# Performance work log

Measured on AMD Instinct MI355X. Metric: run time of the kernel, lower is better.

The kernel has to match this reference:

```python
import jax, jax.numpy as jnp
import numpy as np

N_NODES = 100000
N_EDGES = 1600000
N_QUERY = 200000
IN_CH = 128
HID = 64


def setup_inputs() -> dict:
    key = jax.random.key(0)
    ks = jax.random.split(key, 8)
    x = jax.random.normal(ks[0], (N_NODES, IN_CH), dtype=jnp.float32)
    edge_index = jax.random.randint(ks[1], (2, N_EDGES), 0, N_NODES, dtype=jnp.int64)
    src = jax.random.randint(ks[2], (N_QUERY,), 0, N_NODES, dtype=jnp.int64)
    dst = jax.random.randint(ks[3], (N_QUERY,), 0, N_NODES, dtype=jnp.int64)
    # SAGEConv params: lin_l (neighbor path, with bias), lin_r (root path, no bias)
    s1 = 1.0 / np.sqrt(IN_CH)
    s2 = 1.0 / np.sqrt(HID)
    Wl1 = jax.random.normal(ks[4], (HID, IN_CH), dtype=jnp.float32) * s1
    bl1 = jnp.zeros((HID,), dtype=jnp.float32)
    Wr1 = jax.random.normal(ks[5], (HID, IN_CH), dtype=jnp.float32) * s1
    Wl2 = jax.random.normal(ks[6], (HID, HID), dtype=jnp.float32) * s2
    bl2 = jnp.zeros((HID,), dtype=jnp.float32)
    Wr2 = jax.random.normal(ks[7], (HID, HID), dtype=jnp.float32) * s2
    return {"x": x, "edge_index": edge_index, "src": src, "dst": dst,
            "Wl1": Wl1, "bl1": bl1, "Wr1": Wr1,
            "Wl2": Wl2, "bl2": bl2, "Wr2": Wr2}


def _sage_conv(h, edge_src, edge_dst, Wl, bl, Wr, num_nodes):
    # mean aggregation of source-node features onto destination nodes
    msg_sum = jax.ops.segment_sum(h[edge_src], edge_dst, num_segments=num_nodes)  # [N, F]
    cnt = jax.ops.segment_sum(jnp.ones((edge_src.shape[0], 1), h.dtype), edge_dst,
                              num_segments=num_nodes)  # [N, 1]
    agg = msg_sum / jnp.maximum(cnt, 1.0)
    return agg @ Wl.T + bl + h @ Wr.T


def reference(x, edge_index, src, dst, Wl1, bl1, Wr1, Wl2, bl2, Wr2):
    n = x.shape[0]
    e_src, e_dst = edge_index[0], edge_index[1]
    h = jax.nn.relu(_sage_conv(x, e_src, e_dst, Wl1, bl1, Wr1, n))
    z = jax.nn.relu(_sage_conv(h, e_src, e_dst, Wl2, bl2, Wr2, n))
    return jax.nn.sigmoid(jnp.sum(z[src] * z[dst], axis=-1))
```

## Files before the change

### kernel.cpp

```cpp
#include <hip/hip_runtime.h>
#include <hip/hip_bf16.h>
#include <math.h>


#define HID 64
#define G_BLK 1024
#define NB_MAX 512

typedef __attribute__((ext_vector_type(8))) short short8;
typedef __attribute__((ext_vector_type(4))) float floatx4;

__device__ __forceinline__ unsigned short f2bf(float f) {
    union { float f; unsigned u; } v; v.f = f;
    unsigned r = v.u + 0x7FFF + ((v.u >> 16) & 1);
    return (unsigned short)(r >> 16);
}
__device__ __forceinline__ float bf2f(unsigned short u) {
    union { unsigned u; float f; } v; v.u = ((unsigned)u) << 16;
    return v.f;
}
__device__ __forceinline__ unsigned pack_bf2(float a, float b) {
    union { __hip_bfloat162 h; unsigned u; } cv;
    cv.h = __float22bfloat162_rn(make_float2(a, b));
    return cv.u;
}
__device__ __forceinline__ void acc8(float* a, uint4 u) {
    a[0] += bf2f((unsigned short)u.x); a[1] += bf2f((unsigned short)(u.x >> 16));
    a[2] += bf2f((unsigned short)u.y); a[3] += bf2f((unsigned short)(u.y >> 16));
    a[4] += bf2f((unsigned short)u.z); a[5] += bf2f((unsigned short)(u.z >> 16));
    a[6] += bf2f((unsigned short)u.w); a[7] += bf2f((unsigned short)(u.w >> 16));
}


__global__ __launch_bounds__(256)
void k_bhist(const int* __restrict__ edst, int* __restrict__ cnt,
             int E, int NB, int CH) {
    __shared__ int lh[NB_MAX];
    const int b = blockIdx.x;
    for (int i = threadIdx.x; i < NB; i += 256) lh[i] = 0;
    __syncthreads();
    const int e0 = b * CH;
    const int e1 = min(E, e0 + CH);
    for (int e = e0 + threadIdx.x; e < e1; e += 256)
        atomicAdd(&lh[edst[e] >> 8], 1);
    __syncthreads();
    for (int k = threadIdx.x; k < NB; k += 256)
        cnt[(size_t)k * G_BLK + b] = lh[k];
}

__global__ __launch_bounds__(256)
void k_bscan1(int* __restrict__ cnt, int* __restrict__ total, int NB) {
    int k = blockIdx.x * 4 + (threadIdx.x >> 6);
    int lane = threadIdx.x & 63;
    if (k >= NB) return;
    int* row = cnt + (size_t)k * G_BLK;
    const int base = lane * 16;
    int v[16];
#pragma unroll
    for (int j = 0; j < 16; ++j) v[j] = row[base + j];
    int s = 0;
#pragma unroll
    for (int j = 0; j < 16; ++j) s += v[j];
    int inc = s;
#pragma unroll
    for (int off = 1; off < 64; off <<= 1) {
        int o = __shfl_up(inc, off, 64);
        if (lane >= off) inc += o;
    }
    int run = inc - s;
#pragma unroll
    for (int j = 0; j < 16; ++j) { int t = v[j]; row[base + j] = run; run += t; }
    if (lane == 63) total[k] = run;
}

__global__ __launch_bounds__(512)
void k_bscan2(const int* __restrict__ total, int* __restrict__ base, int NB) {
    __shared__ int lds[512];
    int t = threadIdx.x;
    int v = (t < NB) ? total[t] : 0;
    lds[t] = v;
    __syncthreads();
    for (int off = 1; off < 512; off <<= 1) {
        int x = (t >= off) ? lds[t - off] : 0;
        __syncthreads();
        lds[t] += x;
        __syncthreads();
    }
    if (t < NB) base[t] = lds[t] - v;
}

__global__ __launch_bounds__(256)
void k_bscatter(const int* __restrict__ esrc, const int* __restrict__ edst,
                const int* __restrict__ cnt, const int* __restrict__ base,
                int* __restrict__ ebuf, int E, int NB, int CH) {
    __shared__ int cur[NB_MAX];
    const int b = blockIdx.x;
    for (int k = threadIdx.x; k < NB; k += 256)
        cur[k] = base[k] + cnt[(size_t)k * G_BLK + b];
    __syncthreads();
    const int e0 = b * CH;
    const int e1 = min(E, e0 + CH);
    for (int e = e0 + threadIdx.x; e < e1; e += 256) {
        int d = edst[e];
        int slot = atomicAdd(&cur[d >> 8], 1);
        ebuf[slot] = ((d & 255) << 24) | esrc[e];
    }
}

__global__ __launch_bounds__(256)
void k_bfinal(const int* __restrict__ ebuf, const int* __restrict__ total,
              const int* __restrict__ base, int* __restrict__ sorted,
              int* __restrict__ deg, int* __restrict__ offs, int N) {
    __shared__ int h[256], loc[256], cur[256], sc[256];
    const int k = blockIdx.x;
    const int t = threadIdx.x;
    const int nk = total[k];
    const int bs = base[k];
    h[t] = 0;
    __syncthreads();
    for (int i = bs + t; i < bs + nk; i += 256)
        atomicAdd(&h[(ebuf[i] >> 24) & 255], 1);
    __syncthreads();
    int v = h[t];
    sc[t] = v;
    __syncthreads();
    for (int off = 1; off < 256; off <<= 1) {
        int x = (t >= off) ? sc[t - off] : 0;
        __syncthreads();
        sc[t] += x;
        __syncthreads();
    }
    loc[t] = sc[t] - v;
    cur[t] = sc[t] - v;
    __syncthreads();
    for (int i = bs + t; i < bs + nk; i += 256) {
        int pk = ebuf[i];
        int j = (pk >> 24) & 255;
        int r = atomicAdd(&cur[j], 1);
        sorted[bs + r] = pk & 0xFFFFFF;
    }
    int node = (k << 8) + t;
    if (node < N) {
        deg[node] = v;
        offs[node] = bs + loc[t];
    }
}


template <int K, bool AF32>
__global__ __launch_bounds__(256, 2)
void gemm_mfma(const void* __restrict__ Xv, const float* __restrict__ Wl,
               const float* __restrict__ Wr, unsigned short* __restrict__ Pb,
               unsigned short* __restrict__ Qb, int N) {
    const int lane = threadIdx.x & 63;
    const int m = lane & 15;
    const int q = lane >> 4;
    const int gw = blockIdx.x * 4 + (threadIdx.x >> 6);
    const int half = gw & 1;
    constexpr int KB = K / 32;

    const float* Wh = half ? Wr : Wl;
    short8 bf[KB][4];
#pragma unroll
    for (int kb = 0; kb < KB; ++kb)
#pragma unroll
        for (int ct = 0; ct < 4; ++ct) {
            int c = ct * 16 + m;
            const float* wp = Wh + (size_t)c * K + kb * 32 + q * 8;
            float4 w0 = *(const float4*)wp;
            float4 w1 = *(const float4*)(wp + 4);
            union { unsigned u[4]; short8 s; } cv;
            cv.u[0] = pack_bf2(w0.x, w0.y);
            cv.u[1] = pack_bf2(w0.z, w0.w);
            cv.u[2] = pack_bf2(w1.x, w1.y);
            cv.u[3] = pack_bf2(w1.z, w1.w);
            bf[kb][ct] = cv.s;
        }

    unsigned short* dstp = half ? Qb : Pb;
    const int ntiles = (N + 15) >> 4;
    const int stride = gridDim.x * 2;
    for (int t = gw >> 1; t < ntiles; t += stride) {
        const int r0 = t << 4;
        int rr = r0 + m;
        if (rr >= N) rr = N - 1;
        floatx4 acc[4];
#pragma unroll
        for (int ct = 0; ct < 4; ++ct) acc[ct] = (floatx4){0.f, 0.f, 0.f, 0.f};

#pragma unroll
        for (int kb = 0; kb < KB; ++kb) {
            short8 a;
            if (AF32) {
                const float* xp = (const float*)Xv + (size_t)rr * K + kb * 32 + q * 8;
                float4 x0 = *(const float4*)xp;
                float4 x1 = *(const float4*)(xp + 4);
                union { unsigned u[4]; short8 s; } cv;
                cv.u[0] = pack_bf2(x0.x, x0.y);
                cv.u[1] = pack_bf2(x0.z, x0.w);
                cv.u[2] = pack_bf2(x1.x, x1.y);
                cv.u[3] = pack_bf2(x1.z, x1.w);
                a = cv.s;
            } else {
                a = *(const short8*)((const unsigned short*)Xv + (size_t)rr * K + kb * 32 + q * 8);
            }
#pragma unroll
            for (int ct = 0; ct < 4; ++ct)
                acc[ct] = __builtin_amdgcn_mfma_f32_16x16x32_bf16(a, bf[kb][ct], acc[ct], 0, 0, 0);
        }

#pragma unroll
        for (int i = 0; i < 4; ++i) {
            int row = r0 + q * 4 + i;
            if (row < N) {
#pragma unroll
                for (int ct = 0; ct < 4; ++ct)
                    dstp[(size_t)row * HID + ct * 16 + m] = f2bf(acc[ct][i]);
            }
        }
    }
}


__global__ __launch_bounds__(256)
void k_agg(const uint4* __restrict__ P8, const uint2* __restrict__ Qb4,
           const float4* __restrict__ bias4, const int* __restrict__ offs,
           const int* __restrict__ deg, const int* __restrict__ sorted,
           uint4* __restrict__ H8, int N) {
    int node = blockIdx.x * 32 + (threadIdx.x >> 3);
    int c8 = threadIdx.x & 7;
    if (node >= N) return;
    int off = offs[node];
    int c = deg[node];
    float a[8];
#pragma unroll
    for (int j = 0; j < 8; ++j) a[j] = 0.f;
    int i = 0;
    for (; i + 1 < c; i += 2) {
        int s0 = sorted[off + i];
        int s1 = sorted[off + i + 1];
        uint4 u0 = P8[(size_t)s0 * 8 + c8];
        uint4 u1 = P8[(size_t)s1 * 8 + c8];
        acc8(a, u0);
        acc8(a, u1);
    }
    if (i < c) acc8(a, P8[(size_t)sorted[off + i] * 8 + c8]);

    float inv = 1.0f / (float)(c > 0 ? c : 1);
    float4 b0 = bias4[c8 * 2], b1 = bias4[c8 * 2 + 1];
    uint2 q0 = Qb4[(size_t)node * 16 + c8 * 2];
    uint2 q1 = Qb4[(size_t)node * 16 + c8 * 2 + 1];
    float v0 = a[0] * inv + b0.x + bf2f((unsigned short)q0.x);
    float v1 = a[1] * inv + b0.y + bf2f((unsigned short)(q0.x >> 16));
    float v2 = a[2] * inv + b0.z + bf2f((unsigned short)q0.y);
    float v3 = a[3] * inv + b0.w + bf2f((unsigned short)(q0.y >> 16));
    float v4 = a[4] * inv + b1.x + bf2f((unsigned short)q1.x);
    float v5 = a[5] * inv + b1.y + bf2f((unsigned short)(q1.x >> 16));
    float v6 = a[6] * inv + b1.z + bf2f((unsigned short)q1.y);
    float v7 = a[7] * inv + b1.w + bf2f((unsigned short)(q1.y >> 16));
    v0 = fmaxf(v0, 0.f); v1 = fmaxf(v1, 0.f); v2 = fmaxf(v2, 0.f); v3 = fmaxf(v3, 0.f);
    v4 = fmaxf(v4, 0.f); v5 = fmaxf(v5, 0.f); v6 = fmaxf(v6, 0.f); v7 = fmaxf(v7, 0.f);
    uint4 hp;
    hp.x = (unsigned)f2bf(v0) | ((unsigned)f2bf(v1) << 16);
    hp.y = (unsigned)f2bf(v2) | ((unsigned)f2bf(v3) << 16);
    hp.z = (unsigned)f2bf(v4) | ((unsigned)f2bf(v5) << 16);
    hp.w = (unsigned)f2bf(v6) | ((unsigned)f2bf(v7) << 16);
    H8[(size_t)node * 8 + c8] = hp;
}


__global__ __launch_bounds__(256)
void k_query(const uint4* __restrict__ Z8, const int* __restrict__ src,
             const int* __restrict__ dst, float* __restrict__ out, int Q) {
    int qi = blockIdx.x * 32 + (threadIdx.x >> 3);
    int c8 = threadIdx.x & 7;
    if (qi >= Q) return;
    int s = src[qi];
    int d = dst[qi];
    uint4 us = Z8[(size_t)s * 8 + c8];
    uint4 ud = Z8[(size_t)d * 8 + c8];
    float v =
        bf2f((unsigned short)us.x) * bf2f((unsigned short)ud.x) +
        bf2f((unsigned short)(us.x >> 16)) * bf2f((unsigned short)(ud.x >> 16)) +
        bf2f((unsigned short)us.y) * bf2f((unsigned short)ud.y) +
        bf2f((unsigned short)(us.y >> 16)) * bf2f((unsigned short)(ud.y >> 16)) +
        bf2f((unsigned short)us.z) * bf2f((unsigned short)ud.z) +
        bf2f((unsigned short)(us.z >> 16)) * bf2f((unsigned short)(ud.z >> 16)) +
        bf2f((unsigned short)us.w) * bf2f((unsigned short)ud.w) +
        bf2f((unsigned short)(us.w >> 16)) * bf2f((unsigned short)(ud.w >> 16));
#pragma unroll
    for (int mres = 4; mres > 0; mres >>= 1) v += __shfl_xor(v, mres, 64);
    if (c8 == 0) out[qi] = 1.0f / (1.0f + __expf(-v));
}


extern "C" void kernel_launch(void* const* d_in, const int* in_sizes, int n_in,
                              void* d_out, int out_size, void* d_ws, size_t ws_size,
                              hipStream_t stream) {
    const float* x    = (const float*)d_in[0];
    const int*   ei   = (const int*)d_in[1];
    const int*   qsrc = (const int*)d_in[2];
    const int*   qdst = (const int*)d_in[3];
    const float* Wl1  = (const float*)d_in[4];
    const float* bl1  = (const float*)d_in[5];
    const float* Wr1  = (const float*)d_in[6];
    const float* Wl2  = (const float*)d_in[7];
    const float* bl2  = (const float*)d_in[8];
    const float* Wr2  = (const float*)d_in[9];
    float* out = (float*)d_out;

    const int N = in_sizes[0] / 128;
    const int E = in_sizes[1] / 2;
    const int Q = in_sizes[2];

    const int* esrc = ei;
    const int* edst = ei + E;

    unsigned short* Pb = (unsigned short*)d_ws;
    unsigned short* Qb = Pb + (size_t)N * HID;
    unsigned short* Hb = Qb + (size_t)N * HID;
    unsigned short* Zb = Hb + (size_t)N * HID;
    int* deg_c  = (int*)(Zb + (size_t)N * HID);
    int* offs   = deg_c + N;
    int* total  = offs + N;
    int* base   = total + NB_MAX;
    int* sorted = base + NB_MAX;
    int* cnt    = sorted + E;
    int* ebuf   = cnt + (size_t)NB_MAX * G_BLK;

    const int NB = (N + 255) >> 8;
    const int CH = (E + G_BLK - 1) / G_BLK;
    const int gG = 640;
    const int gA = (N + 31) / 32;
    const int gQ = (Q + 31) / 32;

    k_bhist<<<G_BLK, 256, 0, stream>>>(edst, cnt, E, NB, CH);
    k_bscan1<<<(NB + 3) / 4, 256, 0, stream>>>(cnt, total, NB);
    k_bscan2<<<1, 512, 0, stream>>>(total, base, NB);
    k_bscatter<<<G_BLK, 256, 0, stream>>>(esrc, edst, cnt, base, ebuf, E, NB, CH);
    k_bfinal<<<NB, 256, 0, stream>>>(ebuf, total, base, sorted, deg_c, offs, N);

    gemm_mfma<128, true><<<gG, 256, 0, stream>>>(x, Wl1, Wr1, Pb, Qb, N);
    k_agg<<<gA, 256, 0, stream>>>((const uint4*)Pb, (const uint2*)Qb,
                                  (const float4*)bl1, offs, deg_c, sorted,
                                  (uint4*)Hb, N);

    gemm_mfma<64, false><<<gG, 256, 0, stream>>>(Hb, Wl2, Wr2, Pb, Qb, N);
    k_agg<<<gA, 256, 0, stream>>>((const uint4*)Pb, (const uint2*)Qb,
                                  (const float4*)bl2, offs, deg_c, sorted,
                                  (uint4*)Zb, N);

    k_query<<<gQ, 256, 0, stream>>>((const uint4*)Zb, qsrc, qdst, out, Q);
}
```

Before: 264.1 us.

## Halve histogram grid, unroll aggregation by four, use packed bf16 conversions

Halves the number of histogram blocks used for the bucket sort and shrinks the per-lane scan width to match. The neighbor aggregation loop now issues four gathers per iteration instead of two, raising memory-level parallelism. Bf16 unpacking and packing now go through the paired bfloat162 intrinsics, and the query dot product uses paired FMA chains. The bigger unroll may cost registers, and fewer histogram blocks means more edges handled per block.

```diff
diff --git a/kernel.cpp b/kernel.cpp
--- a/kernel.cpp
+++ b/kernel.cpp
@@ -4,7 +4,7 @@
 
 
 #define HID 64
-#define G_BLK 1024
+#define G_BLK 512
 #define NB_MAX 512
 
 typedef __attribute__((ext_vector_type(8))) short short8;
@@ -24,11 +24,16 @@
     cv.h = __float22bfloat162_rn(make_float2(a, b));
     return cv.u;
 }
-__device__ __forceinline__ void acc8(float* a, uint4 u) {
-    a[0] += bf2f((unsigned short)u.x); a[1] += bf2f((unsigned short)(u.x >> 16));
-    a[2] += bf2f((unsigned short)u.y); a[3] += bf2f((unsigned short)(u.y >> 16));
-    a[4] += bf2f((unsigned short)u.z); a[5] += bf2f((unsigned short)(u.z >> 16));
-    a[6] += bf2f((unsigned short)u.w); a[7] += bf2f((unsigned short)(u.w >> 16));
+__device__ __forceinline__ float2 bfx2(unsigned u) {
+    union { unsigned u; __hip_bfloat162 h; } cv; cv.u = u;
+    return __bfloat1622float2(cv.h);
+}
+__device__ __forceinline__ void accp(float2* a, uint4 u) {
+    float2 f0 = bfx2(u.x), f1 = bfx2(u.y), f2 = bfx2(u.z), f3 = bfx2(u.w);
+    a[0].x += f0.x; a[0].y += f0.y;
+    a[1].x += f1.x; a[1].y += f1.y;
+    a[2].x += f2.x; a[2].y += f2.y;
+    a[3].x += f3.x; a[3].y += f3.y;
 }
 
 
@@ -54,13 +59,13 @@
     int lane = threadIdx.x & 63;
     if (k >= NB) return;
     int* row = cnt + (size_t)k * G_BLK;
-    const int base = lane * 16;
-    int v[16];
-#pragma unroll
-    for (int j = 0; j < 16; ++j) v[j] = row[base + j];
+    const int base = lane * 8;
+    int v[8];
+#pragma unroll
+    for (int j = 0; j < 8; ++j) v[j] = row[base + j];
     int s = 0;
 #pragma unroll
-    for (int j = 0; j < 16; ++j) s += v[j];
+    for (int j = 0; j < 8; ++j) s += v[j];
     int inc = s;
 #pragma unroll
     for (int off = 1; off < 64; off <<= 1) {
@@ -69,7 +74,7 @@
     }
     int run = inc - s;
 #pragma unroll
-    for (int j = 0; j < 16; ++j) { int t = v[j]; row[base + j] = run; run += t; }
+    for (int j = 0; j < 8; ++j) { int t = v[j]; row[base + j] = run; run += t; }
     if (lane == 63) total[k] = run;
 }
 
@@ -232,39 +237,43 @@
     if (node >= N) return;
     int off = offs[node];
     int c = deg[node];
-    float a[8];
-#pragma unroll
-    for (int j = 0; j < 8; ++j) a[j] = 0.f;
+    float2 a[4];
+#pragma unroll
+    for (int j = 0; j < 4; ++j) a[j] = make_float2(0.f, 0.f);
     int i = 0;
-    for (; i + 1 < c; i += 2) {
+    for (; i + 3 < c; i += 4) {
         int s0 = sorted[off + i];
         int s1 = sorted[off + i + 1];
+        int s2 = sorted[off + i + 2];
+        int s3 = sorted[off + i + 3];
         uint4 u0 = P8[(size_t)s0 * 8 + c8];
         uint4 u1 = P8[(size_t)s1 * 8 + c8];
-        acc8(a, u0);
-        acc8(a, u1);
-    }
-    if (i < c) acc8(a, P8[(size_t)sorted[off + i] * 8 + c8]);
+        uint4 u2 = P8[(size_t)s2 * 8 + c8];
+        uint4 u3 = P8[(size_t)s3 * 8 + c8];
+        accp(a, u0); accp(a, u1); accp(a, u2); accp(a, u3);
+    }
+    for (; i < c; ++i) accp(a, P8[(size_t)sorted[off + i] * 8 + c8]);
 
     float inv = 1.0f / (float)(c > 0 ? c : 1);
     float4 b0 = bias4[c8 * 2], b1 = bias4[c8 * 2 + 1];
     uint2 q0 = Qb4[(size_t)node * 16 + c8 * 2];
     uint2 q1 = Qb4[(size_t)node * 16 + c8 * 2 + 1];
-    float v0 = a[0] * inv + b0.x + bf2f((unsigned short)q0.x);
-    float v1 = a[1] * inv + b0.y + bf2f((unsigned short)(q0.x >> 16));
-    float v2 = a[2] * inv + b0.z + bf2f((unsigned short)q0.y);
-    float v3 = a[3] * inv + b0.w + bf2f((unsigned short)(q0.y >> 16));
-    float v4 = a[4] * inv + b1.x + bf2f((unsigned short)q1.x);
-    float v5 = a[5] * inv + b1.y + bf2f((unsigned short)(q1.x >> 16));
-    float v6 = a[6] * inv + b1.z + bf2f((unsigned short)q1.y);
-    float v7 = a[7] * inv + b1.w + bf2f((unsigned short)(q1.y >> 16));
+    float2 r0 = bfx2(q0.x), r1 = bfx2(q0.y), r2 = bfx2(q1.x), r3 = bfx2(q1.y);
+    float v0 = a[0].x * inv + b0.x + r0.x;
+    float v1 = a[0].y * inv + b0.y + r0.y;
+    float v2 = a[1].x * inv + b0.z + r1.x;
+    float v3 = a[1].y * inv + b0.w + r1.y;
+    float v4 = a[2].x * inv + b1.x + r2.x;
+    float v5 = a[2].y * inv + b1.y + r2.y;
+    float v6 = a[3].x * inv + b1.z + r3.x;
+    float v7 = a[3].y * inv + b1.w + r3.y;
     v0 = fmaxf(v0, 0.f); v1 = fmaxf(v1, 0.f); v2 = fmaxf(v2, 0.f); v3 = fmaxf(v3, 0.f);
     v4 = fmaxf(v4, 0.f); v5 = fmaxf(v5, 0.f); v6 = fmaxf(v6, 0.f); v7 = fmaxf(v7, 0.f);
     uint4 hp;
-    hp.x = (unsigned)f2bf(v0) | ((unsigned)f2bf(v1) << 16);
-    hp.y = (unsigned)f2bf(v2) | ((unsigned)f2bf(v3) << 16);
-    hp.z = (unsigned)f2bf(v4) | ((unsigned)f2bf(v5) << 16);
-    hp.w = (unsigned)f2bf(v6) | ((unsigned)f2bf(v7) << 16);
+    hp.x = pack_bf2(v0, v1);
+    hp.y = pack_bf2(v2, v3);
+    hp.z = pack_bf2(v4, v5);
+    hp.w = pack_bf2(v6, v7);
     H8[(size_t)node * 8 + c8] = hp;
 }
 
@@ -279,15 +288,13 @@
     int d = dst[qi];
     uint4 us = Z8[(size_t)s * 8 + c8];
     uint4 ud = Z8[(size_t)d * 8 + c8];
-    float v =
-        bf2f((unsigned short)us.x) * bf2f((unsigned short)ud.x) +
-        bf2f((unsigned short)(us.x >> 16)) * bf2f((unsigned short)(ud.x >> 16)) +
-        bf2f((unsigned short)us.y) * bf2f((unsigned short)ud.y) +
-        bf2f((unsigned short)(us.y >> 16)) * bf2f((unsigned short)(ud.y >> 16)) +
-        bf2f((unsigned short)us.z) * bf2f((unsigned short)ud.z) +
-        bf2f((unsigned short)(us.z >> 16)) * bf2f((unsigned short)(ud.z >> 16)) +
-        bf2f((unsigned short)us.w) * bf2f((unsigned short)ud.w) +
-        bf2f((unsigned short)(us.w >> 16)) * bf2f((unsigned short)(ud.w >> 16));
+    float2 p0 = bfx2(us.x), p1 = bfx2(us.y), p2 = bfx2(us.z), p3 = bfx2(us.w);
+    float2 t0 = bfx2(ud.x), t1 = bfx2(ud.y), t2 = bfx2(ud.z), t3 = bfx2(ud.w);
+    float2 acc2 = make_float2(p0.x * t0.x, p0.y * t0.y);
+    acc2.x = fmaf(p1.x, t1.x, acc2.x); acc2.y = fmaf(p1.y, t1.y, acc2.y);
+    acc2.x = fmaf(p2.x, t2.x, acc2.x); acc2.y = fmaf(p2.y, t2.y, acc2.y);
+    acc2.x = fmaf(p3.x, t3.x, acc2.x); acc2.y = fmaf(p3.y, t3.y, acc2.y);
+    float v = acc2.x + acc2.y;
 #pragma unroll
     for (int mres = 4; mres > 0; mres >>= 1) v += __shfl_xor(v, mres, 64);
     if (c8 == 0) out[qi] = 1.0f / (1.0f + __expf(-v));
```

New measurement: 255.8 us. 1.03x faster.
